# Kernel optimization log

Hardware: AMD Instinct MI355X
Metric: run time of the kernel (lower is better)

Reference implementation:

```python
import jax, jax.numpy as jnp
import numpy as np

ITERS = 10  # resonator iterations (iterations=10 in init_kwargs)

def _bipolar(key, shape):
    return jnp.where(jax.random.normal(key, shape) >= 0, 1.0, -1.0).astype(jnp.float32)

def setup_inputs() -> dict:
    key = jax.random.key(0)
    k1, k2, k3 = jax.random.split(key, 3)
    b, f, v, d = 64, 4, 256, 16384
    input_ = _bipolar(k1, (b, d))
    init_estimates = _bipolar(k2, (b, f, d))
    codebooks = _bipolar(k3, (f, v, d))
    return {"input": input_, "init_estimates": init_estimates, "codebooks": codebooks}

def _sign(x):
    # multiset quantize: bipolar sign (ties -> +1), matching MAP-VSA quantization
    return jnp.where(x >= 0, 1.0, -1.0).astype(x.dtype)

def reference(input, init_estimates, codebooks):
    """CONCURRENT resonator, SOFTWARE mode, activation=NONE, stoch=NONE.
    input: (b, d) bipolar; init_estimates: (b, f, d); codebooks: (f, v, d).
    For bipolar vectors: bind = elementwise *, inverse = identity, so
    multibind of all-but-factor-j equals (product over all f) * estimate_j
    (since e*e = 1). This replaces the roll+stack+multibind with one fused pass.
    """
    def step(est, _):
        total = jnp.prod(est, axis=-2, keepdims=True)        # (b, 1, d)
        inv_others = total * est                             # (b, f, d) product of other factors
        new_est = input[:, None, :] * inv_others             # unbind: (b, f, d)
        sim = jnp.einsum('bfd,fvd->bfv', new_est, codebooks) # dot_similarity
        # multiset(codebook, similarity, quantize=True): sign of similarity-weighted sum
        est_new = _sign(jnp.einsum('bfv,fvd->bfd', sim, codebooks))
        return est_new, None
    est, _ = jax.lax.scan(step, init_estimates, None, length=ITERS)
    # cleanup: argmax of |similarity| per factor (argmax_abs=True)
    sim = jnp.einsum('bfd,fvd->bfv', est, codebooks)
    outcome = jnp.argmax(jnp.abs(sim), axis=-1)              # (b, f) codeword indices
    return est, outcome
```

## Files before the change

kernel.cpp:

```cpp
#include <hip/hip_runtime.h>
#include <stdint.h>

typedef unsigned long long ull;
typedef unsigned int u32;
typedef __attribute__((ext_vector_type(8))) short bf16x8;
typedef __attribute__((ext_vector_type(4))) float f32x4;


#define AS __HIP_MEMORY_SCOPE_AGENT
__device__ __forceinline__ ull ald(const ull* p) {
    return __hip_atomic_load(p, __ATOMIC_RELAXED, AS);
}
__device__ __forceinline__ void ast(ull* p, ull v) {
    __hip_atomic_store(p, v, __ATOMIC_RELAXED, AS);
}
__device__ __forceinline__ u32 ald32(const u32* p) {
    return __hip_atomic_load(p, __ATOMIC_RELAXED, AS);
}
__device__ __forceinline__ void ast32(u32* p, u32 v) {
    __hip_atomic_store(p, v, __ATOMIC_RELAXED, AS);
}

__global__ __launch_bounds__(1024) void pack_mega(
        const float* __restrict__ in, const float* __restrict__ est_f,
        const float* __restrict__ cb,
        ull* __restrict__ in_bits, ull* __restrict__ est_bits, ull* __restrict__ cbw,
        ull* __restrict__ bar) {
    if (blockIdx.x == 0 && threadIdx.x < 64) bar[threadIdx.x] = 0;
    int wid  = (int)((blockIdx.x * 1024 + threadIdx.x) >> 6);
    int lane = threadIdx.x & 63;
    int w0 = wid * 16;
    const float* s;
    int wloc;
    if (w0 < 16384)      { s = in;    wloc = w0; }
    else if (w0 < 81920) { s = est_f; wloc = w0 - 16384; }
    else                 { s = cb;    wloc = w0 - 81920; }
    ull ball[16];
    #pragma unroll
    for (int k = 0; k < 16; ++k) {
        float x = s[(size_t)(wloc + k) * 64 + lane];
        ball[k] = __ballot(x < 0.0f);
    }
    if (lane == 0) {
        if (w0 < 16384) {
            #pragma unroll
            for (int k = 0; k < 16; ++k) in_bits[wloc + k] = ball[k];
        } else if (w0 < 81920) {
            #pragma unroll
            for (int k = 0; k < 16; ++k) est_bits[wloc + k] = ball[k];
        } else {
            #pragma unroll
            for (int k = 0; k < 16; ++k) {
                int g = wloc + k;
                int f = g >> 16, v = (g >> 8) & 255, w = g & 255;
                cbw[(size_t)(f * 256 + w) * 256 + v] = ball[k];
            }
        }
    }
}

__global__ __launch_bounds__(1024) void pack_cbT(const ull* __restrict__ cbw, ull* __restrict__ cbT) {
    int wid  = (int)((blockIdx.x * 1024 + threadIdx.x) >> 6);
    int lane = threadIdx.x & 63;
    int f = wid >> 12, j = (wid >> 10) & 3, w = (wid >> 2) & 255, s2 = wid & 3;
    ull cw = cbw[(size_t)(f * 256 + w) * 256 + j * 64 + lane];
    ull ball[16];
    #pragma unroll
    for (int k = 0; k < 16; ++k)
        ball[k] = __ballot((cw >> (s2 * 16 + k)) & 1ull);
    if (lane == 0) {
        #pragma unroll
        for (int k = 0; k < 16; ++k)
            cbT[(size_t)(f * 4 + j) * 16384 + w * 64 + s2 * 16 + k] = ball[k];
    }
}

__global__ __launch_bounds__(512) void reso_kernel(
        const ull* __restrict__ in_bits, ull* __restrict__ est0, ull* __restrict__ est1,
        const ull* __restrict__ cbw, const ull* __restrict__ cbT,
        u32* __restrict__ simAB, ull* __restrict__ bar, float* __restrict__ out) {
    __shared__ __align__(16) char smraw[143360];
    ull  (*s_cw)[64]     = (ull (*)[64])smraw;
    ull  (*s_ne)[256]    = (ull (*)[256])(smraw + 131072);
    short (*s_p)[8][64]  = (short (*)[8][64])(smraw + 139264);
    int4* sB             = (int4*)smraw;
    ull  (*s_ball)[8][4] = (ull (*)[8][4])(smraw + 131072);

    int t = threadIdx.x, lane = t & 63, wave = t >> 6;
    int bid = blockIdx.x;
    int f    = (bid & 7) >> 1;
    int sub  = (bid & 1) * 32 + (bid >> 3);
    int vblk = sub & 3, bblk = sub >> 2;
    int dblk = sub;

    #pragma unroll 4
    for (int i = 0; i < 16; ++i) {
        int idx = i * 1024 + t * 2;
        int w = idx >> 6, v = idx & 63;
        *(ulonglong2*)&s_cw[w][v] =
            *(const ulonglong2*)&cbw[(size_t)(f * 256 + w) * 256 + vblk * 64 + v];
    }

    for (int itr = 0; itr <= 10; ++itr) {
        ull* estIn  = (itr & 1) ? est1 : est0;
        ull* estOut = (itr & 1) ? est0 : est1;
        const int mode = (itr == 10);

        #pragma unroll
        for (int i = 0; i < 2; ++i) {
            int idx = i * 512 + t;
            int bl = idx >> 8, w = idx & 255;
            int b = bblk * 4 + bl;
            ull e0 = ald(&estIn[(size_t)(b * 4 + 0) * 256 + w]);
            ull e1 = ald(&estIn[(size_t)(b * 4 + 1) * 256 + w]);
            ull e2 = ald(&estIn[(size_t)(b * 4 + 2) * 256 + w]);
            ull e3 = ald(&estIn[(size_t)(b * 4 + 3) * 256 + w]);
            ull ef = (f == 0) ? e0 : ((f == 1) ? e1 : ((f == 2) ? e2 : e3));
            s_ne[bl][w] = mode ? ef : (in_bits[(size_t)b * 256 + w] ^ e0 ^ e1 ^ e2 ^ e3 ^ ef);
        }
        __syncthreads();
        {
            int acc0 = 0, acc1 = 0, acc2 = 0, acc3 = 0;
            #pragma unroll 8
            for (int w = wave * 32; w < wave * 32 + 32; ++w) {
                ull cwv = s_cw[w][lane];
                acc0 += __popcll(s_ne[0][w] ^ cwv);
                acc1 += __popcll(s_ne[1][w] ^ cwv);
                acc2 += __popcll(s_ne[2][w] ^ cwv);
                acc3 += __popcll(s_ne[3][w] ^ cwv);
            }
            s_p[0][wave][lane] = (short)acc0;
            s_p[1][wave][lane] = (short)acc1;
            s_p[2][wave][lane] = (short)acc2;
            s_p[3][wave][lane] = (short)acc3;
        }
        __syncthreads();
        if (t < 256) {
            int bi = t >> 6, v2 = t & 63;
            int h = 0;
            #pragma unroll
            for (int c = 0; c < 8; ++c) h += s_p[bi][c][v2];
            int b = bblk * 4 + bi, v = vblk * 64 + v2;
            u32 val;
            if (!mode) {
                int sim = 16384 - 2 * h;
                int sh = sim >> 8, sl = sim & 255;
                val = (u32)(__float_as_uint((float)sh) >> 16)
                    | ((u32)(__float_as_uint((float)sl) >> 16) << 16);
            } else {
                val = (u32)(16384 - h);
            }
            ast32(&simAB[((size_t)(f * 64 + b) << 8) + v], val);
        }
        __syncthreads();
        if (t == 0) atomicAdd(&bar[itr * 2], 1ull);
        if (!mode) {
            #pragma unroll 4
            for (int it2 = 0; it2 < 16; ++it2) {
                int flat = it2 * 512 + t;
                int kc = flat >> 10, nt = (flat >> 6) & 15, l = flat & 63;
                int v0 = kc * 32 + ((l >> 4) << 3);
                int d  = dblk * 256 + nt * 16 + (l & 15);
                ull w = cbT[((size_t)f * 4 + (v0 >> 6)) * 16384 + d];
                unsigned bits = (unsigned)(w >> (v0 & 63)) & 0xFFu;
                int4 valB;
                valB.x = 0x3F803F80 | ((bits & 1u) << 15)        | ((bits & 2u) << 30);
                valB.y = 0x3F803F80 | (((bits >> 2) & 1u) << 15) | (((bits >> 2) & 2u) << 30);
                valB.z = 0x3F803F80 | (((bits >> 4) & 1u) << 15) | (((bits >> 4) & 2u) << 30);
                valB.w = 0x3F803F80 | (((bits >> 6) & 1u) << 15) | (((bits >> 6) & 2u) << 30);
                sB[flat] = valB;
            }
        }
        if (t == 0) { while (ald(&bar[itr * 2]) < 256ull) __builtin_amdgcn_s_sleep(1); }
        __syncthreads();
        if (mode) break;

        int mw = wave & 3, ntb = (wave >> 2) << 3;
        const ull* ab = (const ull*)(simAB + (((size_t)(f * 64 + mw * 16 + (lane & 15))) << 8))
                        + ((lane >> 4) << 2);
        bf16x8 Ahi[8], Alo[8];
        #pragma unroll
        for (int kc = 0; kc < 8; ++kc) {
            union { u32 u[4]; bf16x8 v; } H, L;
            #pragma unroll
            for (int p2 = 0; p2 < 4; ++p2) {
                ull w = ald(ab + kc * 16 + p2);
                H.u[p2] = (u32)(w & 0xFFFFull) | (((u32)(w >> 32) & 0xFFFFu) << 16);
                L.u[p2] = ((u32)(w >> 16) & 0xFFFFu) | ((u32)(w >> 48) << 16);
            }
            Ahi[kc] = H.v; Alo[kc] = L.v;
        }
        #pragma unroll 2
        for (int ntl = 0; ntl < 8; ++ntl) {
            int nt = ntb + ntl;
            f32x4 acch = {0.f, 0.f, 0.f, 0.f}, accl = {0.f, 0.f, 0.f, 0.f};
            #pragma unroll
            for (int kc = 0; kc < 8; ++kc) {
                bf16x8 B = *(const bf16x8*)&sB[(kc * 16 + nt) * 64 + lane];
                acch = __builtin_amdgcn_mfma_f32_16x16x32_bf16(Ahi[kc], B, acch, 0, 0, 0);
                accl = __builtin_amdgcn_mfma_f32_16x16x32_bf16(Alo[kc], B, accl, 0, 0, 0);
            }
            #pragma unroll
            for (int r = 0; r < 4; ++r) {
                float S = 256.0f * acch[r] + accl[r];
                ull m = __ballot(S < 0.0f);
                if (lane == 0) s_ball[wave][nt & 7][r] = m;
            }
        }
        __syncthreads();
        if (t < 256) {
            int b = t >> 2, w4 = t & 3;
            int wv = (b >> 4) + ((w4 >= 2) ? 4 : 0);
            ull word = 0;
            #pragma unroll
            for (int k = 0; k < 4; ++k) {
                int nt = w4 * 4 + k;
                ull m = s_ball[wv][nt & 7][b & 3];
                word |= ((m >> (((b >> 2) & 3) * 16)) & 0xFFFFull) << (k * 16);
            }
            ast(&estOut[((size_t)(b * 4 + f)) * 256 + dblk * 4 + w4], word);
        }
        __syncthreads();
        if (t == 0) atomicAdd(&bar[itr * 2 + 1], 1ull);
        #pragma unroll 4
        for (int i = 0; i < 16; ++i) {
            int idx = i * 1024 + t * 2;
            int w = idx >> 6, v = idx & 63;
            *(ulonglong2*)&s_cw[w][v] =
                *(const ulonglong2*)&cbw[(size_t)(f * 256 + w) * 256 + vblk * 64 + v];
        }
        if (t == 0) { while (ald(&bar[itr * 2 + 1]) < 256ull) __builtin_amdgcn_s_sleep(1); }
        __syncthreads();
    }

    if (t < 64) {
        int b2 = bid >> 2, f2 = bid & 3;
        const ull* sf = (const ull*)(simAB + ((size_t)(f2 * 64 + b2) << 8)) + t * 2;
        ull w0 = ald(sf), w1 = ald(sf + 1);
        int qv[4] = { (int)(u32)w0, (int)(u32)(w0 >> 32),
                      (int)(u32)w1, (int)(u32)(w1 >> 32) };
        int best_a = -1, best_v = 0;
        #pragma unroll
        for (int k = 0; k < 4; ++k) {
            int sim = 2 * qv[k] - 16384;
            int a = sim < 0 ? -sim : sim;
            if (a > best_a) { best_a = a; best_v = t * 4 + k; }
        }
        #pragma unroll
        for (int off = 1; off < 64; off <<= 1) {
            int oa = __shfl_xor(best_a, off);
            int ov = __shfl_xor(best_v, off);
            if (oa > best_a || (oa == best_a && ov < best_v)) { best_a = oa; best_v = ov; }
        }
        if (t == 0) out[4194304 + b2 * 4 + f2] = (float)best_v;
    }
    {
        int widx = bid * 256 + (t >> 1);
        ull w = ald(&est0[widx]);
        u32 bits = (u32)(w >> ((t & 1) * 32));
        int base = bid * 16384 + (t >> 1) * 64 + (t & 1) * 32;
        #pragma unroll
        for (int j = 0; j < 8; ++j) {
            float4 o;
            o.x = ((bits >> (j * 4 + 0)) & 1u) ? -1.0f : 1.0f;
            o.y = ((bits >> (j * 4 + 1)) & 1u) ? -1.0f : 1.0f;
            o.z = ((bits >> (j * 4 + 2)) & 1u) ? -1.0f : 1.0f;
            o.w = ((bits >> (j * 4 + 3)) & 1u) ? -1.0f : 1.0f;
            *(float4*)(out + base + j * 4) = o;
        }
    }
}

extern "C" void kernel_launch(void* const* d_in, const int* in_sizes, int n_in,
                              void* d_out, int out_size, void* d_ws, size_t ws_size,
                              hipStream_t stream) {
    const float* input    = (const float*)d_in[0];
    const float* init_est = (const float*)d_in[1];
    const float* cb       = (const float*)d_in[2];
    float* out = (float*)d_out;
    char* ws = (char*)d_ws;

    ull* in_bits = (ull*)(ws + 0);
    ull* est0    = (ull*)(ws + 131072);
    ull* est1    = (ull*)(ws + 655360);
    ull* cbw     = (ull*)(ws + 1179648);
    ull* cbT     = (ull*)(ws + 3276800);
    u32* simAB   = (u32*)(ws + 5373952);
    ull* bar     = (ull*)(ws + 5636096);

    pack_mega<<<1344, 1024, 0, stream>>>(input, init_est, cb, in_bits, est0, cbw, bar);
    pack_cbT<<<1024, 1024, 0, stream>>>(cbw, cbT);

    void* kargs[] = {
        (void*)&in_bits, (void*)&est0, (void*)&est1, (void*)&cbw, (void*)&cbT,
        (void*)&simAB, (void*)&bar, (void*)&out
    };
    hipLaunchCooperativeKernel(reinterpret_cast<void*>(reso_kernel),
                               dim3(256, 1, 1), dim3(512, 1, 1), kargs, 0, stream);
}
```

Measured before the change: 391.6 us.

## Keep codebook resident in LDS, double threads, flag-based grid barrier, readlane popcount

Raises the block size to 1024 threads and keeps the codebook slice in a swizzled LDS layout for the whole run, so it is no longer reloaded every iteration. The bit-packed transposed codebook is cached once in LDS and expanded to bf16 MFMA operands in registers, replacing the per-iteration sB staging from global memory. The unbound estimate is broadcast with readlane instead of being staged in LDS. The grid barrier changes from shared atomic counters to per-block monotonic flags polled by 256 threads, and simAB is written in an MFMA-friendly layout so A-operand loads coalesce. In exchange it adds register pressure at 1024 threads and more LDS traffic.

New measurement: 432.7 us. 10.5% more time.

```diff
diff --git a/kernel.cpp b/kernel.cpp
--- a/kernel.cpp
+++ b/kernel.cpp
@@ -13,9 +13,6 @@
 }
 __device__ __forceinline__ void ast(ull* p, ull v) {
     __hip_atomic_store(p, v, __ATOMIC_RELAXED, AS);
-}
-__device__ __forceinline__ u32 ald32(const u32* p) {
-    return __hip_atomic_load(p, __ATOMIC_RELAXED, AS);
 }
 __device__ __forceinline__ void ast32(u32* p, u32 v) {
     __hip_atomic_store(p, v, __ATOMIC_RELAXED, AS);
@@ -26,7 +23,7 @@
         const float* __restrict__ cb,
         ull* __restrict__ in_bits, ull* __restrict__ est_bits, ull* __restrict__ cbw,
         ull* __restrict__ bar) {
-    if (blockIdx.x == 0 && threadIdx.x < 64) bar[threadIdx.x] = 0;
+    if (blockIdx.x == 0 && threadIdx.x < 256) bar[threadIdx.x] = 0;
     int wid  = (int)((blockIdx.x * 1024 + threadIdx.x) >> 6);
     int lane = threadIdx.x & 63;
     int w0 = wid * 16;
@@ -75,16 +72,15 @@
     }
 }
 
-__global__ __launch_bounds__(512) void reso_kernel(
+__global__ __launch_bounds__(1024) void reso_kernel(
         const ull* __restrict__ in_bits, ull* __restrict__ est0, ull* __restrict__ est1,
         const ull* __restrict__ cbw, const ull* __restrict__ cbT,
         u32* __restrict__ simAB, ull* __restrict__ bar, float* __restrict__ out) {
-    __shared__ __align__(16) char smraw[143360];
-    ull  (*s_cw)[64]     = (ull (*)[64])smraw;
-    ull  (*s_ne)[256]    = (ull (*)[256])(smraw + 131072);
-    short (*s_p)[8][64]  = (short (*)[8][64])(smraw + 139264);
-    int4* sB             = (int4*)smraw;
-    ull  (*s_ball)[8][4] = (ull (*)[8][4])(smraw + 131072);
+    __shared__ __align__(16) char smraw[149504];
+    ull*   s_cw   = (ull*)smraw;
+    ull*   s_bT   = (ull*)(smraw + 131072);
+    short* s_p    = (short*)(smraw + 139264);
+    ull*   s_ball = (ull*)(smraw + 147456);
 
     int t = threadIdx.x, lane = t & 63, wave = t >> 6;
     int bid = blockIdx.x;
@@ -95,141 +91,139 @@
 
     #pragma unroll 4
     for (int i = 0; i < 16; ++i) {
-        int idx = i * 1024 + t * 2;
-        int w = idx >> 6, v = idx & 63;
-        *(ulonglong2*)&s_cw[w][v] =
-            *(const ulonglong2*)&cbw[(size_t)(f * 256 + w) * 256 + vblk * 64 + v];
-    }
-
+        int idx = i * 1024 + t;
+        int v = idx & 63, w = idx >> 6;
+        s_cw[(v * 128 + ((w >> 1) ^ (v & 7))) * 2 + (w & 1)] =
+            cbw[(size_t)(f * 256 + w) * 256 + vblk * 64 + v];
+    }
+    s_bT[t] = cbT[((size_t)f * 4 + (t >> 8)) * 16384 + dblk * 256 + (t & 255)];
+    __syncthreads();
+
+    int tag = 0;
     for (int itr = 0; itr <= 10; ++itr) {
         ull* estIn  = (itr & 1) ? est1 : est0;
         ull* estOut = (itr & 1) ? est0 : est1;
-        const int mode = (itr == 10);
-
-        #pragma unroll
-        for (int i = 0; i < 2; ++i) {
-            int idx = i * 512 + t;
-            int bl = idx >> 8, w = idx & 255;
-            int b = bblk * 4 + bl;
-            ull e0 = ald(&estIn[(size_t)(b * 4 + 0) * 256 + w]);
-            ull e1 = ald(&estIn[(size_t)(b * 4 + 1) * 256 + w]);
-            ull e2 = ald(&estIn[(size_t)(b * 4 + 2) * 256 + w]);
-            ull e3 = ald(&estIn[(size_t)(b * 4 + 3) * 256 + w]);
+        const bool mode1 = (itr == 10);
+
+        {
+            int bA = bblk * 4 + (lane >> 4);
+            int wA = wave * 16 + (lane & 15);
+            ull e0 = ald(&estIn[(size_t)(bA * 4 + 0) * 256 + wA]);
+            ull e1 = ald(&estIn[(size_t)(bA * 4 + 1) * 256 + wA]);
+            ull e2 = ald(&estIn[(size_t)(bA * 4 + 2) * 256 + wA]);
+            ull e3 = ald(&estIn[(size_t)(bA * 4 + 3) * 256 + wA]);
             ull ef = (f == 0) ? e0 : ((f == 1) ? e1 : ((f == 2) ? e2 : e3));
-            s_ne[bl][w] = mode ? ef : (in_bits[(size_t)b * 256 + w] ^ e0 ^ e1 ^ e2 ^ e3 ^ ef);
-        }
-        __syncthreads();
-        {
+            ull ne = mode1 ? ef : (in_bits[(size_t)bA * 256 + wA] ^ e0 ^ e1 ^ e2 ^ e3 ^ ef);
+            u32 ne_lo = (u32)ne, ne_hi = (u32)(ne >> 32);
+
             int acc0 = 0, acc1 = 0, acc2 = 0, acc3 = 0;
-            #pragma unroll 8
-            for (int w = wave * 32; w < wave * 32 + 32; ++w) {
-                ull cwv = s_cw[w][lane];
-                acc0 += __popcll(s_ne[0][w] ^ cwv);
-                acc1 += __popcll(s_ne[1][w] ^ cwv);
-                acc2 += __popcll(s_ne[2][w] ^ cwv);
-                acc3 += __popcll(s_ne[3][w] ^ cwv);
-            }
-            s_p[0][wave][lane] = (short)acc0;
-            s_p[1][wave][lane] = (short)acc1;
-            s_p[2][wave][lane] = (short)acc2;
-            s_p[3][wave][lane] = (short)acc3;
+            #pragma unroll
+            for (int it = 0; it < 8; ++it) {
+                int wp = wave * 8 + it;
+                const ulonglong2 cw =
+                    *(const ulonglong2*)&s_cw[(lane * 128 + (wp ^ (lane & 7))) * 2];
+                u32 cxl = (u32)cw.x, cxh = (u32)(cw.x >> 32);
+                u32 cyl = (u32)cw.y, cyh = (u32)(cw.y >> 32);
+                #pragma unroll
+                for (int bi = 0; bi < 4; ++bi) {
+                    const int s0 = bi * 16 + it * 2;
+                    u32 a0 = __builtin_amdgcn_readlane(ne_lo, s0);
+                    u32 a1 = __builtin_amdgcn_readlane(ne_hi, s0);
+                    u32 b0 = __builtin_amdgcn_readlane(ne_lo, s0 + 1);
+                    u32 b1 = __builtin_amdgcn_readlane(ne_hi, s0 + 1);
+                    int p = __builtin_popcount(cxl ^ a0) + __builtin_popcount(cxh ^ a1)
+                          + __builtin_popcount(cyl ^ b0) + __builtin_popcount(cyh ^ b1);
+                    if (bi == 0) acc0 += p; else if (bi == 1) acc1 += p;
+                    else if (bi == 2) acc2 += p; else acc3 += p;
+                }
+            }
+            s_p[(0 * 16 + wave) * 64 + lane] = (short)acc0;
+            s_p[(1 * 16 + wave) * 64 + lane] = (short)acc1;
+            s_p[(2 * 16 + wave) * 64 + lane] = (short)acc2;
+            s_p[(3 * 16 + wave) * 64 + lane] = (short)acc3;
         }
         __syncthreads();
         if (t < 256) {
             int bi = t >> 6, v2 = t & 63;
             int h = 0;
             #pragma unroll
-            for (int c = 0; c < 8; ++c) h += s_p[bi][c][v2];
+            for (int q = 0; q < 16; ++q) h += s_p[(bi * 16 + q) * 64 + v2];
             int b = bblk * 4 + bi, v = vblk * 64 + v2;
-            u32 val;
-            if (!mode) {
+            if (!mode1) {
                 int sim = 16384 - 2 * h;
                 int sh = sim >> 8, sl = sim & 255;
-                val = (u32)(__float_as_uint((float)sh) >> 16)
-                    | ((u32)(__float_as_uint((float)sl) >> 16) << 16);
+                u32 val = (u32)(__float_as_uint((float)sh) >> 16)
+                        | ((u32)(__float_as_uint((float)sl) >> 16) << 16);
+                int mw = b >> 4, brow = b & 15;
+                int kc = v >> 5, kgrp = (v >> 3) & 3, j = v & 7;
+                int uidx = ((((mw * 8 + kc) * 4 + (j >> 1)) * 64) + kgrp * 16 + brow) * 2 + (j & 1);
+                ast32(&simAB[f * 16384 + uidx], val);
             } else {
-                val = (u32)(16384 - h);
-            }
-            ast32(&simAB[((size_t)(f * 64 + b) << 8) + v], val);
-        }
-        __syncthreads();
-        if (t == 0) atomicAdd(&bar[itr * 2], 1ull);
-        if (!mode) {
-            #pragma unroll 4
-            for (int it2 = 0; it2 < 16; ++it2) {
-                int flat = it2 * 512 + t;
-                int kc = flat >> 10, nt = (flat >> 6) & 15, l = flat & 63;
-                int v0 = kc * 32 + ((l >> 4) << 3);
-                int d  = dblk * 256 + nt * 16 + (l & 15);
-                ull w = cbT[((size_t)f * 4 + (v0 >> 6)) * 16384 + d];
-                unsigned bits = (unsigned)(w >> (v0 & 63)) & 0xFFu;
-                int4 valB;
-                valB.x = 0x3F803F80 | ((bits & 1u) << 15)        | ((bits & 2u) << 30);
-                valB.y = 0x3F803F80 | (((bits >> 2) & 1u) << 15) | (((bits >> 2) & 2u) << 30);
-                valB.z = 0x3F803F80 | (((bits >> 4) & 1u) << 15) | (((bits >> 4) & 2u) << 30);
-                valB.w = 0x3F803F80 | (((bits >> 6) & 1u) << 15) | (((bits >> 6) & 2u) << 30);
-                sB[flat] = valB;
-            }
-        }
-        if (t == 0) { while (ald(&bar[itr * 2]) < 256ull) __builtin_amdgcn_s_sleep(1); }
-        __syncthreads();
-        if (mode) break;
-
-        int mw = wave & 3, ntb = (wave >> 2) << 3;
-        const ull* ab = (const ull*)(simAB + (((size_t)(f * 64 + mw * 16 + (lane & 15))) << 8))
-                        + ((lane >> 4) << 2);
-        bf16x8 Ahi[8], Alo[8];
-        #pragma unroll
-        for (int kc = 0; kc < 8; ++kc) {
-            union { u32 u[4]; bf16x8 v; } H, L;
-            #pragma unroll
-            for (int p2 = 0; p2 < 4; ++p2) {
-                ull w = ald(ab + kc * 16 + p2);
-                H.u[p2] = (u32)(w & 0xFFFFull) | (((u32)(w >> 32) & 0xFFFFu) << 16);
-                L.u[p2] = ((u32)(w >> 16) & 0xFFFFu) | ((u32)(w >> 48) << 16);
-            }
-            Ahi[kc] = H.v; Alo[kc] = L.v;
-        }
-        #pragma unroll 2
-        for (int ntl = 0; ntl < 8; ++ntl) {
-            int nt = ntb + ntl;
-            f32x4 acch = {0.f, 0.f, 0.f, 0.f}, accl = {0.f, 0.f, 0.f, 0.f};
+                ast32(&simAB[((f * 64 + b) << 8) + v], (u32)(16384 - h));
+            }
+        }
+        __syncthreads();
+        ++tag;
+        if (t == 0) ast(&bar[bid], (ull)tag);
+        if (t < 256) { while (ald(&bar[t]) < (ull)tag) __builtin_amdgcn_s_sleep(1); }
+        __syncthreads();
+        if (mode1) break;
+
+        {
+            int mw = wave & 3, qtr = wave >> 2;
+            const ull* ab8 = (const ull*)simAB + (size_t)f * 8192;
+            bf16x8 Ahi[8], Alo[8];
             #pragma unroll
             for (int kc = 0; kc < 8; ++kc) {
-                bf16x8 B = *(const bf16x8*)&sB[(kc * 16 + nt) * 64 + lane];
-                acch = __builtin_amdgcn_mfma_f32_16x16x32_bf16(Ahi[kc], B, acch, 0, 0, 0);
-                accl = __builtin_amdgcn_mfma_f32_16x16x32_bf16(Alo[kc], B, accl, 0, 0, 0);
-            }
-            #pragma unroll
-            for (int r = 0; r < 4; ++r) {
-                float S = 256.0f * acch[r] + accl[r];
-                ull m = __ballot(S < 0.0f);
-                if (lane == 0) s_ball[wave][nt & 7][r] = m;
+                union { u32 u[4]; bf16x8 v; } H, L;
+                #pragma unroll
+                for (int n = 0; n < 4; ++n) {
+                    ull w = ald(ab8 + (((mw * 8 + kc) * 4 + n) * 64) + lane);
+                    H.u[n] = (u32)(w & 0xFFFFull) | (((u32)(w >> 32) & 0xFFFFu) << 16);
+                    L.u[n] = ((u32)(w >> 16) & 0xFFFFu) | ((u32)(w >> 48) << 16);
+                }
+                Ahi[kc] = H.v; Alo[kc] = L.v;
+            }
+            #pragma unroll
+            for (int ntl = 0; ntl < 4; ++ntl) {
+                int nt = qtr * 4 + ntl;
+                f32x4 acch = {0.f, 0.f, 0.f, 0.f}, accl = {0.f, 0.f, 0.f, 0.f};
+                #pragma unroll
+                for (int kc = 0; kc < 8; ++kc) {
+                    ull w = s_bT[(kc >> 1) * 256 + nt * 16 + (lane & 15)];
+                    u32 bits = (u32)(w >> ((kc & 1) * 32 + (lane >> 4) * 8)) & 0xFFu;
+                    union { u32 u[4]; bf16x8 v; } B;
+                    B.u[0] = 0x3F803F80 | ((bits & 1u) << 15)        | ((bits & 2u) << 30);
+                    B.u[1] = 0x3F803F80 | (((bits >> 2) & 1u) << 15) | (((bits >> 2) & 2u) << 30);
+                    B.u[2] = 0x3F803F80 | (((bits >> 4) & 1u) << 15) | (((bits >> 4) & 2u) << 30);
+                    B.u[3] = 0x3F803F80 | (((bits >> 6) & 1u) << 15) | (((bits >> 6) & 2u) << 30);
+                    acch = __builtin_amdgcn_mfma_f32_16x16x32_bf16(Ahi[kc], B.v, acch, 0, 0, 0);
+                    accl = __builtin_amdgcn_mfma_f32_16x16x32_bf16(Alo[kc], B.v, accl, 0, 0, 0);
+                }
+                #pragma unroll
+                for (int r = 0; r < 4; ++r) {
+                    float S = 256.0f * acch[r] + accl[r];
+                    ull m = __ballot(S < 0.0f);
+                    if (lane == 0) s_ball[(wave * 4 + ntl) * 4 + r] = m;
+                }
             }
         }
         __syncthreads();
         if (t < 256) {
             int b = t >> 2, w4 = t & 3;
-            int wv = (b >> 4) + ((w4 >= 2) ? 4 : 0);
+            int wv = (w4 << 2) | (b >> 4);
             ull word = 0;
             #pragma unroll
             for (int k = 0; k < 4; ++k) {
-                int nt = w4 * 4 + k;
-                ull m = s_ball[wv][nt & 7][b & 3];
+                ull m = s_ball[(wv * 4 + k) * 4 + (b & 3)];
                 word |= ((m >> (((b >> 2) & 3) * 16)) & 0xFFFFull) << (k * 16);
             }
             ast(&estOut[((size_t)(b * 4 + f)) * 256 + dblk * 4 + w4], word);
         }
         __syncthreads();
-        if (t == 0) atomicAdd(&bar[itr * 2 + 1], 1ull);
-        #pragma unroll 4
-        for (int i = 0; i < 16; ++i) {
-            int idx = i * 1024 + t * 2;
-            int w = idx >> 6, v = idx & 63;
-            *(ulonglong2*)&s_cw[w][v] =
-                *(const ulonglong2*)&cbw[(size_t)(f * 256 + w) * 256 + vblk * 64 + v];
-        }
-        if (t == 0) { while (ald(&bar[itr * 2 + 1]) < 256ull) __builtin_amdgcn_s_sleep(1); }
+        ++tag;
+        if (t == 0) ast(&bar[bid], (ull)tag);
+        if (t < 256) { while (ald(&bar[t]) < (ull)tag) __builtin_amdgcn_s_sleep(1); }
         __syncthreads();
     }
 
@@ -255,12 +249,11 @@
         if (t == 0) out[4194304 + b2 * 4 + f2] = (float)best_v;
     }
     {
-        int widx = bid * 256 + (t >> 1);
-        ull w = ald(&est0[widx]);
-        u32 bits = (u32)(w >> ((t & 1) * 32));
-        int base = bid * 16384 + (t >> 1) * 64 + (t & 1) * 32;
-        #pragma unroll
-        for (int j = 0; j < 8; ++j) {
+        ull w = ald(&est0[bid * 256 + (t >> 2)]);
+        u32 bits = (u32)(w >> ((t & 3) * 16)) & 0xFFFFu;
+        int base = bid * 16384 + (t >> 2) * 64 + (t & 3) * 16;
+        #pragma unroll
+        for (int j = 0; j < 4; ++j) {
             float4 o;
             o.x = ((bits >> (j * 4 + 0)) & 1u) ? -1.0f : 1.0f;
             o.y = ((bits >> (j * 4 + 1)) & 1u) ? -1.0f : 1.0f;
@@ -296,5 +289,5 @@
         (void*)&simAB, (void*)&bar, (void*)&out
     };
     hipLaunchCooperativeKernel(reinterpret_cast<void*>(reso_kernel),
-                               dim3(256, 1, 1), dim3(512, 1, 1), kargs, 0, stream);
-}
+                               dim3(256, 1, 1), dim3(1024, 1, 1), kargs, 0, stream);
+}
```
